# Optimization experiments

Hardware: AMD Instinct MI355X
Metric: run time of the kernel (lower is better)

Reference implementation:

```python
import jax, jax.numpy as jnp
import numpy as np

EMB = 1024
HEADS = 16


def setup_inputs() -> dict:
    key = jax.random.key(0)
    ks = jax.random.split(key, 5)
    s = 1.0 / np.sqrt(EMB).astype(np.float32)
    return {
        "x": jax.random.normal(ks[0], (4, 2048, EMB), dtype=jnp.float32),
        "Wq": jax.random.normal(ks[1], (EMB, EMB), dtype=jnp.float32) * s,
        "bq": jnp.zeros((EMB,), dtype=jnp.float32),
        "Wk": jax.random.normal(ks[2], (EMB, EMB), dtype=jnp.float32) * s,
        "bk": jnp.zeros((EMB,), dtype=jnp.float32),
        "Wv": jax.random.normal(ks[3], (EMB, EMB), dtype=jnp.float32) * s,
        "bv": jnp.zeros((EMB,), dtype=jnp.float32),
        "Wo": jax.random.normal(ks[4], (EMB, EMB), dtype=jnp.float32) * s,
        "bo": jnp.zeros((EMB,), dtype=jnp.float32),
    }


def reference(x, Wq, bq, Wk, bk, Wv, bv, Wo, bo):
    b, n, e = x.shape
    h = HEADS
    d = e // h
    # QKV projections, split heads: [b, n, e] -> [b, h, n, d]
    def split_heads(t):
        return t.reshape(b, n, h, d).transpose(0, 2, 1, 3)
    q = split_heads(x @ Wq + bq)
    k = split_heads(x @ Wk + bk)
    v = split_heads(x @ Wv + bv)
    # NOTE: original scales by sqrt(emb_size), not sqrt(head_dim)
    energy = jnp.einsum('bhqd,bhkd->bhqk', q, k)
    att = jax.nn.softmax(energy / jnp.sqrt(jnp.float32(e)), axis=-1)
    # dropout is identity in eval mode
    out = jnp.einsum('bhqk,bhkd->bhqd', att, v)
    out = out.transpose(0, 2, 1, 3).reshape(b, n, e)
    return out @ Wo + bo
```

## Files before the change

kernel.cpp:

```cpp
#include <hip/hip_runtime.h>

#define EMB   1024
#define SEQ   2048
#define BATCH 4
#define HEADS 16
#define HDIM  64
#define MTOT  8192

typedef __bf16 bf16x8 __attribute__((ext_vector_type(8)));
typedef float  fx4    __attribute__((ext_vector_type(4)));

#if __has_builtin(__builtin_amdgcn_exp2f)
#define EXP2(x) __builtin_amdgcn_exp2f(x)
#else
#define EXP2(x) exp2f(x)
#endif

__device__ __forceinline__ unsigned short f2bf(float f) {
    unsigned u = __builtin_bit_cast(unsigned, f);
    u += 0x7fffu + ((u >> 16) & 1u);
    return (unsigned short)(u >> 16);
}
__device__ __forceinline__ unsigned short bfbits(float f) {
    __bf16 h = (__bf16)f;
    return __builtin_bit_cast(unsigned short, h);
}

#define AS1 __attribute__((address_space(1)))
#define AS3 __attribute__((address_space(3)))
__device__ __forceinline__ void glds16(const void* g, void* l) {
    __builtin_amdgcn_global_load_lds((AS1 void*)g, (AS3 void*)l, 16, 0, 0);
}
#define DRAIN_GLDS() __builtin_amdgcn_s_waitcnt(0x0f70)

#define QSCALE 0.0450842137604569f

__global__ __launch_bounds__(256) void cvt_x_kernel(const float* __restrict__ x,
                                                    unsigned short* __restrict__ xb)
{
    const int idx = (blockIdx.x * 256 + threadIdx.x) * 4;
    const float4 v = *(const float4*)(x + idx);
    ushort4 o;
    o.x = f2bf(v.x); o.y = f2bf(v.y); o.z = f2bf(v.z); o.w = f2bf(v.w);
    *(ushort4*)(xb + idx) = o;
}

__global__ __launch_bounds__(256) void cvt_w_kernel(
    const float* __restrict__ w0, const float* __restrict__ w1,
    const float* __restrict__ w2, const float* __restrict__ w3,
    unsigned short* __restrict__ o0, unsigned short* __restrict__ o1,
    unsigned short* __restrict__ o2, unsigned short* __restrict__ o3)
{
    const int z = blockIdx.z;
    const float* W = z == 0 ? w0 : (z == 1 ? w1 : (z == 2 ? w2 : w3));
    unsigned short* O = z == 0 ? o0 : (z == 1 ? o1 : (z == 2 ? o2 : o3));

    __shared__ float Ws[64][65];
    const int t  = threadIdx.x;
    const int k0 = blockIdx.x * 64, n0 = blockIdx.y * 64;
#pragma unroll
    for (int p = 0; p < 4; ++p) {
        const int row = p * 16 + (t >> 4);
        const int col = (t & 15) * 4;
        const float4 v = *(const float4*)(W + (size_t)(k0 + row) * EMB + n0 + col);
        Ws[row][col]     = v.x; Ws[row][col + 1] = v.y;
        Ws[row][col + 2] = v.z; Ws[row][col + 3] = v.w;
    }
    __syncthreads();
    const int nn = t >> 2;
    const int kb = (t & 3) * 16;
#pragma unroll
    for (int q = 0; q < 2; ++q) {
        const int kk = kb + q * 8;
        ushort4 u0, u1;
        u0.x = f2bf(Ws[kk + 0][nn]); u0.y = f2bf(Ws[kk + 1][nn]);
        u0.z = f2bf(Ws[kk + 2][nn]); u0.w = f2bf(Ws[kk + 3][nn]);
        u1.x = f2bf(Ws[kk + 4][nn]); u1.y = f2bf(Ws[kk + 5][nn]);
        u1.z = f2bf(Ws[kk + 6][nn]); u1.w = f2bf(Ws[kk + 7][nn]);
        *(ushort4*)(O + (size_t)(n0 + nn) * EMB + k0 + kk)     = u0;
        *(ushort4*)(O + (size_t)(n0 + nn) * EMB + k0 + kk + 4) = u1;
    }
}

__global__ __launch_bounds__(256) void gemm_bf16_kernel(
    const unsigned short* __restrict__ Ag,
    const unsigned short* __restrict__ B0, const unsigned short* __restrict__ B1,
    const unsigned short* __restrict__ B2,
    const float* __restrict__ bias0, const float* __restrict__ bias1,
    const float* __restrict__ bias2,
    void* out0, void* out1, void* out2, int mode)
{
    const int z = blockIdx.z;
    const unsigned short* __restrict__ Bg = z == 0 ? B0 : (z == 1 ? B1 : B2);
    const float* __restrict__ bias = z == 0 ? bias0 : (z == 1 ? bias1 : bias2);
    void* outp = z == 0 ? out0 : (z == 1 ? out1 : out2);

    __shared__ unsigned short As[128][32];
    __shared__ unsigned short Bs[128][32];

    const int t    = threadIdx.x;
    const int w    = t >> 6;
    const int lane = t & 63;
    const int low4 = lane & 15;
    const int quad = lane >> 4;
    const int m0 = blockIdx.x * 128;
    const int e0 = blockIdx.y * 128;
    const int we = (w & 1) * 64;
    const int wm = (w >> 1) * 64;

    const int srow = w * 32 + (lane >> 2);
    const int scol = (lane & 3) * 8;

    fx4 acc[4][4] = {};

    for (int k0 = 0; k0 < EMB; k0 += 32) {
        __syncthreads();
        glds16(Ag + (size_t)(m0 + srow) * EMB + k0 + scol,      &As[w * 32][0]);
        glds16(Ag + (size_t)(m0 + srow + 16) * EMB + k0 + scol, &As[w * 32 + 16][0]);
        glds16(Bg + (size_t)(e0 + srow) * EMB + k0 + scol,      &Bs[w * 32][0]);
        glds16(Bg + (size_t)(e0 + srow + 16) * EMB + k0 + scol, &Bs[w * 32 + 16][0]);
        DRAIN_GLDS();
        __syncthreads();

        bf16x8 af[4], bfr[4];
#pragma unroll
        for (int i = 0; i < 4; ++i) {
            af[i]  = *(const bf16x8*)&Bs[we + i * 16 + low4][quad * 8];
            bfr[i] = *(const bf16x8*)&As[wm + i * 16 + low4][quad * 8];
        }
#pragma unroll
        for (int i = 0; i < 4; ++i)
#pragma unroll
            for (int j = 0; j < 4; ++j)
                acc[i][j] = __builtin_amdgcn_mfma_f32_16x16x32_bf16(af[i], bfr[j], acc[i][j], 0, 0, 0);
    }

    fx4 bv[4];
#pragma unroll
    for (int i = 0; i < 4; ++i)
        bv[i] = *(const fx4*)(bias + e0 + we + i * 16 + quad * 4);

#pragma unroll
    for (int i = 0; i < 4; ++i) {
#pragma unroll
        for (int j = 0; j < 4; ++j) {
            const int m  = m0 + wm + j * 16 + low4;
            const int eb = e0 + we + i * 16 + quad * 4;
            if (mode == 1) {
                fx4 o4;
#pragma unroll
                for (int rr = 0; rr < 4; ++rr) o4[rr] = acc[i][j][rr] + bv[i][rr];
                *(fx4*)((float*)outp + (size_t)m * EMB + eb) = o4;
            } else {
                const int bb = m >> 11, n = m & (SEQ - 1);
                const int hh = eb >> 6, db = eb & 63;
                unsigned short* o = (unsigned short*)outp;
                if (z <= 1) {
                    const float sc = (z == 0) ? QSCALE : 1.0f;
                    ushort4 o4;
                    o4.x = f2bf((acc[i][j][0] + bv[i][0]) * sc);
                    o4.y = f2bf((acc[i][j][1] + bv[i][1]) * sc);
                    o4.z = f2bf((acc[i][j][2] + bv[i][2]) * sc);
                    o4.w = f2bf((acc[i][j][3] + bv[i][3]) * sc);
                    *(ushort4*)(o + (((size_t)(bb * HEADS + hh)) * SEQ + n) * HDIM + db) = o4;
                } else {
                    const int nl = n & 63;
                    const int np = (n & ~63) | (((nl & 15) << 2) | (nl >> 4));
#pragma unroll
                    for (int rr = 0; rr < 4; ++rr)
                        o[(((size_t)(bb * HEADS + hh)) * HDIM + db + rr) * SEQ + np] =
                            f2bf(acc[i][j][rr] + bv[i][rr]);
                }
            }
        }
    }
}

__global__ __launch_bounds__(256, 2) void attn_mfma3_kernel(
    const unsigned short* __restrict__ qg, const unsigned short* __restrict__ kg,
    const unsigned short* __restrict__ vg, unsigned short* __restrict__ attb)
{
    __shared__ unsigned short Ks[2][64][64];
    __shared__ unsigned short Vs[2][64][64];
    __shared__ unsigned short Ps[4][16][72];

    const int t    = threadIdx.x;
    const int w    = t >> 6;
    const int lane = t & 63;
    const int low4 = lane & 15;
    const int quad = lane >> 4;
    const int q0   = blockIdx.x * 256 + w * 64;
    const int bh   = blockIdx.y;
    const size_t base = (size_t)bh * SEQ * HDIM;

    const int srow8  = lane >> 3;
    const int schunk = (lane & 7) ^ srow8;

    bf16x8 aq[4][2];
#pragma unroll
    for (int s = 0; s < 4; ++s) {
        const size_t qrow = base + (size_t)(q0 + s * 16 + low4) * HDIM;
        aq[s][0] = *(const bf16x8*)(qg + qrow + quad * 8);
        aq[s][1] = *(const bf16x8*)(qg + qrow + 32 + quad * 8);
    }

    fx4 o_acc[4][4] = {};
    float l_i[4][4] = {};
    const fx4 fzero = {0.f, 0.f, 0.f, 0.f};

    {
        const unsigned short* kp = kg + base + (size_t)(w * 16 + srow8) * HDIM + schunk * 8;
        glds16(kp,              &Ks[0][w * 16][0]);
        glds16(kp + 8 * HDIM,   &Ks[0][w * 16 + 8][0]);
        const unsigned short* vp = vg + base + (size_t)(w * 16 + srow8) * SEQ + schunk * 8;
        glds16(vp,              &Vs[0][w * 16][0]);
        glds16(vp + 8 * SEQ,    &Vs[0][w * 16 + 8][0]);
    }

    for (int tt0 = 0; tt0 < SEQ / 64; ++tt0) {
        const int buf = tt0 & 1;
        DRAIN_GLDS();
        __syncthreads();

        bf16x8 kf[4][2], vf[4][2];
#pragma unroll
        for (int tk = 0; tk < 4; ++tk) {
            const int row = tk * 16 + low4;
            const int x7  = low4 & 7;
#pragma unroll
            for (int c = 0; c < 2; ++c) {
                const int lc = (c * 4 + quad) ^ x7;
                kf[tk][c] = *(const bf16x8*)&Ks[buf][row][lc * 8];
                vf[tk][c] = *(const bf16x8*)&Vs[buf][row][lc * 8];
            }
        }

        if (tt0 + 1 < SEQ / 64) {
            const int kv1 = (tt0 + 1) * 64;
            const unsigned short* kp = kg + base + (size_t)(kv1 + w * 16 + srow8) * HDIM + schunk * 8;
            glds16(kp,            &Ks[buf ^ 1][w * 16][0]);
            glds16(kp + 8 * HDIM, &Ks[buf ^ 1][w * 16 + 8][0]);
            const unsigned short* vp = vg + base + (size_t)(w * 16 + srow8) * SEQ + kv1 + schunk * 8;
            glds16(vp,            &Vs[buf ^ 1][w * 16][0]);
            glds16(vp + 8 * SEQ,  &Vs[buf ^ 1][w * 16 + 8][0]);
        }

#pragma unroll
        for (int s = 0; s < 4; ++s) {
            fx4 sa[4];
#pragma unroll
            for (int tk = 0; tk < 4; ++tk) {
                sa[tk] = __builtin_amdgcn_mfma_f32_16x16x32_bf16(aq[s][0], kf[tk][0], fzero, 0, 0, 0);
                sa[tk] = __builtin_amdgcn_mfma_f32_16x16x32_bf16(aq[s][1], kf[tk][1], sa[tk], 0, 0, 0);
            }
#pragma unroll
            for (int r = 0; r < 4; ++r) {
                const float p0 = EXP2(sa[0][r]);
                const float p1 = EXP2(sa[1][r]);
                const float p2 = EXP2(sa[2][r]);
                const float p3 = EXP2(sa[3][r]);
                l_i[s][r] += (p0 + p1) + (p2 + p3);
                uint2 pk;
                pk.x = (unsigned)bfbits(p0) | ((unsigned)bfbits(p1) << 16);
                pk.y = (unsigned)bfbits(p2) | ((unsigned)bfbits(p3) << 16);
                *(uint2*)&Ps[w][quad * 4 + r][low4 * 4] = pk;
            }
            __asm__ volatile("" ::: "memory");
            bf16x8 pf0 = *(const bf16x8*)&Ps[w][low4][quad * 8];
            bf16x8 pf1 = *(const bf16x8*)&Ps[w][low4][32 + quad * 8];
#pragma unroll
            for (int t2 = 0; t2 < 4; ++t2) {
                o_acc[s][t2] = __builtin_amdgcn_mfma_f32_16x16x32_bf16(pf0, vf[t2][0], o_acc[s][t2], 0, 0, 0);
                o_acc[s][t2] = __builtin_amdgcn_mfma_f32_16x16x32_bf16(pf1, vf[t2][1], o_acc[s][t2], 0, 0, 0);
            }
        }
    }

#pragma unroll
    for (int s = 0; s < 4; ++s)
#pragma unroll
        for (int r = 0; r < 4; ++r) {
            float v = l_i[s][r];
            for (int off = 1; off < 16; off <<= 1)
                v += __shfl_xor(v, off, 16);
            l_i[s][r] = 1.0f / v;
        }

    const int bb = bh >> 4, hh = bh & 15;
#pragma unroll
    for (int s = 0; s < 4; ++s)
#pragma unroll
        for (int r = 0; r < 4; ++r) {
            const size_t m = (size_t)bb * SEQ + q0 + s * 16 + quad * 4 + r;
#pragma unroll
            for (int t2 = 0; t2 < 4; ++t2) {
                const int e = hh * HDIM + t2 * 16 + low4;
                attb[m * EMB + e] = bfbits(o_acc[s][t2][r] * l_i[s][r]);
            }
        }
}

extern "C" void kernel_launch(void* const* d_in, const int* in_sizes, int n_in,
                              void* d_out, int out_size, void* d_ws, size_t ws_size,
                              hipStream_t stream)
{
    const float* x  = (const float*)d_in[0];
    const float* Wq = (const float*)d_in[1];
    const float* bq = (const float*)d_in[2];
    const float* Wk = (const float*)d_in[3];
    const float* bk = (const float*)d_in[4];
    const float* Wv = (const float*)d_in[5];
    const float* bv = (const float*)d_in[6];
    const float* Wo = (const float*)d_in[7];
    const float* bo = (const float*)d_in[8];

    unsigned short* ws  = (unsigned short*)d_ws;
    unsigned short* xb  = ws;
    unsigned short* wqt = xb + 8388608;
    unsigned short* wkt = wqt + 1048576;
    unsigned short* wvt = wkt + 1048576;
    unsigned short* wot = wvt + 1048576;
    unsigned short* qb  = wot + 1048576;
    unsigned short* kbuf = qb + 8388608;
    unsigned short* vtb  = kbuf + 8388608;
    unsigned short* attb = vtb + 8388608;

    cvt_x_kernel<<<8192, 256, 0, stream>>>(x, xb);
    cvt_w_kernel<<<dim3(16, 16, 4), 256, 0, stream>>>(Wq, Wk, Wv, Wo, wqt, wkt, wvt, wot);

    gemm_bf16_kernel<<<dim3(64, 8, 3), 256, 0, stream>>>(
        xb, wqt, wkt, wvt, bq, bk, bv, qb, kbuf, vtb, 0);

    attn_mfma3_kernel<<<dim3(8, 64), 256, 0, stream>>>(qb, kbuf, vtb, attb);

    gemm_bf16_kernel<<<dim3(64, 8, 1), 256, 0, stream>>>(
        attb, wot, wot, wot, bo, bo, bo, d_out, d_out, d_out, 1);
}
```

Baseline: 291.5 us.

## Swizzle GEMM LDS tiles, vectorize V-transpose stores, split P staging per subtile

```diff
diff --git a/kernel.cpp b/kernel.cpp
--- a/kernel.cpp
+++ b/kernel.cpp
@@ -108,8 +108,11 @@
     const int we = (w & 1) * 64;
     const int wm = (w >> 1) * 64;
 
-    const int srow = w * 32 + (lane >> 2);
-    const int scol = (lane & 3) * 8;
+    const int srow   = w * 32 + (lane >> 2);
+    const int schunk = (lane & 3) ^ ((lane >> 3) & 3);
+    const int scol   = schunk * 8;
+
+    const int fchunk = (quad ^ ((low4 >> 1) & 3)) * 8;
 
     fx4 acc[4][4] = {};
 
@@ -125,8 +128,8 @@
         bf16x8 af[4], bfr[4];
 #pragma unroll
         for (int i = 0; i < 4; ++i) {
-            af[i]  = *(const bf16x8*)&Bs[we + i * 16 + low4][quad * 8];
-            bfr[i] = *(const bf16x8*)&As[wm + i * 16 + low4][quad * 8];
+            af[i]  = *(const bf16x8*)&Bs[we + i * 16 + low4][fchunk];
+            bfr[i] = *(const bf16x8*)&As[wm + i * 16 + low4][fchunk];
         }
 #pragma unroll
         for (int i = 0; i < 4; ++i)
@@ -140,49 +143,66 @@
     for (int i = 0; i < 4; ++i)
         bv[i] = *(const fx4*)(bias + e0 + we + i * 16 + quad * 4);
 
-#pragma unroll
-    for (int i = 0; i < 4; ++i) {
-#pragma unroll
-        for (int j = 0; j < 4; ++j) {
-            const int m  = m0 + wm + j * 16 + low4;
-            const int eb = e0 + we + i * 16 + quad * 4;
-            if (mode == 1) {
+    if (mode == 1) {
+#pragma unroll
+        for (int i = 0; i < 4; ++i)
+#pragma unroll
+            for (int j = 0; j < 4; ++j) {
+                const int m  = m0 + wm + j * 16 + low4;
+                const int eb = e0 + we + i * 16 + quad * 4;
                 fx4 o4;
 #pragma unroll
                 for (int rr = 0; rr < 4; ++rr) o4[rr] = acc[i][j][rr] + bv[i][rr];
                 *(fx4*)((float*)outp + (size_t)m * EMB + eb) = o4;
-            } else {
+            }
+    } else if (z <= 1) {
+        const float sc = (z == 0) ? QSCALE : 1.0f;
+        unsigned short* o = (unsigned short*)outp;
+#pragma unroll
+        for (int i = 0; i < 4; ++i)
+#pragma unroll
+            for (int j = 0; j < 4; ++j) {
+                const int m  = m0 + wm + j * 16 + low4;
+                const int eb = e0 + we + i * 16 + quad * 4;
                 const int bb = m >> 11, n = m & (SEQ - 1);
                 const int hh = eb >> 6, db = eb & 63;
-                unsigned short* o = (unsigned short*)outp;
-                if (z <= 1) {
-                    const float sc = (z == 0) ? QSCALE : 1.0f;
-                    ushort4 o4;
-                    o4.x = f2bf((acc[i][j][0] + bv[i][0]) * sc);
-                    o4.y = f2bf((acc[i][j][1] + bv[i][1]) * sc);
-                    o4.z = f2bf((acc[i][j][2] + bv[i][2]) * sc);
-                    o4.w = f2bf((acc[i][j][3] + bv[i][3]) * sc);
-                    *(ushort4*)(o + (((size_t)(bb * HEADS + hh)) * SEQ + n) * HDIM + db) = o4;
-                } else {
-                    const int nl = n & 63;
-                    const int np = (n & ~63) | (((nl & 15) << 2) | (nl >> 4));
-#pragma unroll
-                    for (int rr = 0; rr < 4; ++rr)
-                        o[(((size_t)(bb * HEADS + hh)) * HDIM + db + rr) * SEQ + np] =
-                            f2bf(acc[i][j][rr] + bv[i][rr]);
-                }
-            }
-        }
-    }
-}
-
-__global__ __launch_bounds__(256, 2) void attn_mfma3_kernel(
+                ushort4 o4;
+                o4.x = f2bf((acc[i][j][0] + bv[i][0]) * sc);
+                o4.y = f2bf((acc[i][j][1] + bv[i][1]) * sc);
+                o4.z = f2bf((acc[i][j][2] + bv[i][2]) * sc);
+                o4.w = f2bf((acc[i][j][3] + bv[i][3]) * sc);
+                *(ushort4*)(o + (((size_t)(bb * HEADS + hh)) * SEQ + n) * HDIM + db) = o4;
+            }
+    } else {
+        unsigned short* o = (unsigned short*)outp;
+        const int mbase = m0 + wm;
+        const int bb    = mbase >> 11;
+        const int nb    = mbase & (SEQ - 1);
+#pragma unroll
+        for (int i = 0; i < 4; ++i) {
+            const int eb = e0 + we + i * 16 + quad * 4;
+            const int hh = eb >> 6, db = eb & 63;
+#pragma unroll
+            for (int rr = 0; rr < 4; ++rr) {
+                ushort4 o4;
+                o4.x = f2bf(acc[i][0][rr] + bv[i][rr]);
+                o4.y = f2bf(acc[i][1][rr] + bv[i][rr]);
+                o4.z = f2bf(acc[i][2][rr] + bv[i][rr]);
+                o4.w = f2bf(acc[i][3][rr] + bv[i][rr]);
+                *(ushort4*)(o + (((size_t)(bb * HEADS + hh)) * HDIM + db + rr) * SEQ
+                              + nb + low4 * 4) = o4;
+            }
+        }
+    }
+}
+
+__global__ __launch_bounds__(256, 2) void attn_mfma4_kernel(
     const unsigned short* __restrict__ qg, const unsigned short* __restrict__ kg,
     const unsigned short* __restrict__ vg, unsigned short* __restrict__ attb)
 {
     __shared__ unsigned short Ks[2][64][64];
     __shared__ unsigned short Vs[2][64][64];
-    __shared__ unsigned short Ps[4][16][72];
+    __shared__ unsigned short Ps[4][4][16][72];
 
     const int t    = threadIdx.x;
     const int w    = t >> 6;
@@ -263,11 +283,10 @@
                 uint2 pk;
                 pk.x = (unsigned)bfbits(p0) | ((unsigned)bfbits(p1) << 16);
                 pk.y = (unsigned)bfbits(p2) | ((unsigned)bfbits(p3) << 16);
-                *(uint2*)&Ps[w][quad * 4 + r][low4 * 4] = pk;
-            }
-            __asm__ volatile("" ::: "memory");
-            bf16x8 pf0 = *(const bf16x8*)&Ps[w][low4][quad * 8];
-            bf16x8 pf1 = *(const bf16x8*)&Ps[w][low4][32 + quad * 8];
+                *(uint2*)&Ps[w][s][quad * 4 + r][low4 * 4] = pk;
+            }
+            bf16x8 pf0 = *(const bf16x8*)&Ps[w][s][low4][quad * 8];
+            bf16x8 pf1 = *(const bf16x8*)&Ps[w][s][low4][32 + quad * 8];
 #pragma unroll
             for (int t2 = 0; t2 < 4; ++t2) {
                 o_acc[s][t2] = __builtin_amdgcn_mfma_f32_16x16x32_bf16(pf0, vf[t2][0], o_acc[s][t2], 0, 0, 0);
@@ -331,7 +350,7 @@
     gemm_bf16_kernel<<<dim3(64, 8, 3), 256, 0, stream>>>(
         xb, wqt, wkt, wvt, bq, bk, bv, qb, kbuf, vtb, 0);
 
-    attn_mfma3_kernel<<<dim3(8, 64), 256, 0, stream>>>(qb, kbuf, vtb, attb);
+    attn_mfma4_kernel<<<dim3(8, 64), 256, 0, stream>>>(qb, kbuf, vtb, attb);
 
     gemm_bf16_kernel<<<dim3(64, 8, 1), 256, 0, stream>>>(
         attb, wot, wot, wot, bo, bo, bo, d_out, d_out, d_out, 1);
```

Result: faster. 284.0 us (-2.6%).
